# Performance work log

Hardware: AMD Instinct MI355X
Metric: run time of the kernel (lower is better)

The kernel has to match this reference:

```python
import jax, jax.numpy as jnp
import numpy as np

B, S, D = 4, 2048, 2048
H, K = 16, 128          # num_heads, intermediate_dim
FINAL = H * K           # 2048
VDIM = 2048             # vector_dim
EPS_LN = 1e-6
EPS_NORM = 1e-30


def setup_inputs() -> dict:
    key = jax.random.key(0)
    ks = jax.random.split(key, 8)
    x = jax.random.normal(ks[0], (B, S, D), dtype=jnp.float32)
    vector = jax.random.normal(ks[1], (B, VDIM), dtype=jnp.float32)
    W_att = jax.random.normal(ks[2], (D, H), dtype=jnp.float32) / np.sqrt(D)
    temperature = jnp.ones((1, 1, H), dtype=jnp.float32)
    W_values = jax.random.normal(ks[3], (D, H, K), dtype=jnp.float32) / np.sqrt(D)
    W_op = jax.random.normal(ks[4], (FINAL, VDIM), dtype=jnp.float32) / np.sqrt(FINAL)
    ff1 = jax.random.normal(ks[5], (VDIM + D, D), dtype=jnp.float32) / np.sqrt(VDIM + D)
    ff1_b = jnp.zeros((1, 1, D), dtype=jnp.float32)
    ff2 = jax.random.normal(ks[6], (D, D), dtype=jnp.float32) / np.sqrt(D)
    ff2_b = jnp.zeros((1, 1, D), dtype=jnp.float32)
    gamma = jnp.ones((D,), dtype=jnp.float32)
    beta = jnp.zeros((D,), dtype=jnp.float32)
    return {"x": x, "vector": vector, "W_att": W_att, "temperature": temperature,
            "W_values": W_values, "W_op": W_op, "ff1": ff1, "ff1_b": ff1_b,
            "ff2": ff2, "ff2_b": ff2_b, "gamma": gamma, "beta": beta}


def reference(x, vector, W_att, temperature, W_values, W_op, ff1, ff1_b, ff2, ff2_b, gamma, beta):
    b, s, d = x.shape
    # attention gate per (query) position -- [B,S,H]
    logits = jnp.matmul(x, W_att)
    logits = logits - jnp.max(logits, axis=-2, keepdims=True)
    w = jnp.exp(logits * temperature)
    # exact collapse of repeat+tril+normalize: A[b,i,j,h] = w[b,i,h]*tril[i,j]
    # denom[b,i,h] = w[b,i,h]*(i+1) + 1e-30  ->  out = coef * causal cumsum of v
    counts = jnp.arange(1, s + 1, dtype=x.dtype)[None, :, None]  # [1,S,1]
    coef = w / (w * counts + EPS_NORM)                            # [B,S,H]
    v = jnp.einsum('bsi,ihk->bshk', x, W_values)                  # [B,S,H,K]
    cum_v = jnp.cumsum(v, axis=1)                                 # prefix-sum over keys
    pooled = (coef[..., None] * cum_v).reshape(b, s, -1)          # [B,S,H*K]
    op = jnp.matmul(pooled, W_op) + vector[:, None, :]            # [B,S,VDIM]
    concat = jnp.concatenate([x, op], axis=-1)                    # [B,S,VDIM+D]
    h = jax.nn.relu(jnp.matmul(concat, ff1) + ff1_b)
    h = jax.nn.relu(jnp.matmul(h, ff2) + ff2_b)
    res = h + x
    mean = jnp.mean(res, axis=-1, keepdims=True)
    cen = res - mean
    var = jnp.mean(cen * cen, axis=-1, keepdims=True)
    return cen / jnp.sqrt(var + EPS_LN) * gamma + beta
```

## Files before the change

kernel.cpp:

```cpp
#include <hip/hip_runtime.h>
#include <stdint.h>

#define B_DIM 4
#define S_DIM 2048
#define D_DIM 2048
#define H_DIM 16
#define M_ROWS (B_DIM * S_DIM)
#define CONCAT_LD 4096
#define NCHUNK 32
#define CHLEN (S_DIM / NCHUNK)

#define BM 128
#define BN 128
#define BK 64

typedef __attribute__((ext_vector_type(8))) __bf16 bf16x8;
typedef __attribute__((ext_vector_type(4))) float f32x4;

__device__ inline unsigned short f2bf(float f) {
  union { float f; unsigned u; } x; x.f = f;
  unsigned r = x.u + 0x7fffu + ((x.u >> 16) & 1u);
  return (unsigned short)(r >> 16);
}
__device__ inline float bf2f(unsigned short s) {
  union { unsigned u; float f; } x; x.u = ((unsigned)s) << 16;
  return x.f;
}

__global__ __launch_bounds__(256) void xconv_logits_kernel(
    const float* __restrict__ x, const float* __restrict__ Watt,
    unsigned short* __restrict__ concat, float* __restrict__ logits) {
  int row = blockIdx.x, t = threadIdx.x;
  const float* xr = x + (size_t)row * D_DIM;
  unsigned short* cr = concat + (size_t)row * CONCAT_LD;
  float p[H_DIM];
#pragma unroll
  for (int h = 0; h < H_DIM; ++h) p[h] = 0.f;
#pragma unroll
  for (int i = 0; i < 8; ++i) {
    int k = t + i * 256;
    float xv = xr[k];
    cr[k] = f2bf(xv);
    const float* wr = Watt + (size_t)k * H_DIM;
#pragma unroll
    for (int h = 0; h < H_DIM; ++h) p[h] += xv * wr[h];
  }
  __shared__ float red[4][H_DIM];
  int l = t & 63, w = t >> 6;
#pragma unroll
  for (int h = 0; h < H_DIM; ++h) {
    float v = p[h];
    for (int off = 32; off; off >>= 1) v += __shfl_down(v, off);
    if (l == 0) red[w][h] = v;
  }
  __syncthreads();
  if (t < H_DIM)
    logits[(size_t)row * H_DIM + t] = red[0][t] + red[1][t] + red[2][t] + red[3][t];
}

__global__ __launch_bounds__(256) void transpose_conv_kernel(
    const float* __restrict__ src, unsigned short* __restrict__ dst, int R, int C) {
  __shared__ float tile[32][33];
  int c0 = blockIdx.x * 32, r0 = blockIdx.y * 32;
  int tx = threadIdx.x & 31, ty = threadIdx.x >> 5;
#pragma unroll
  for (int i = 0; i < 32; i += 8)
    tile[ty + i][tx] = src[(size_t)(r0 + ty + i) * C + c0 + tx];
  __syncthreads();
#pragma unroll
  for (int i = 0; i < 32; i += 8)
    dst[(size_t)(c0 + ty + i) * R + r0 + tx] = f2bf(tile[tx][ty + i]);
}

__global__ __launch_bounds__(256) void coef_kernel(
    const float* __restrict__ logits, const float* __restrict__ temp, float* __restrict__ coef) {
  int b = blockIdx.x >> 4, h = blockIdx.x & 15;
  int t = threadIdx.x;
  const float* lg = logits + (size_t)b * S_DIM * H_DIM + h;
  float mx = -1e30f;
  for (int s = t; s < S_DIM; s += 256) mx = fmaxf(mx, lg[(size_t)s * H_DIM]);
  for (int off = 32; off; off >>= 1) mx = fmaxf(mx, __shfl_down(mx, off));
  __shared__ float red[4];
  if ((t & 63) == 0) red[t >> 6] = mx;
  __syncthreads();
  mx = fmaxf(fmaxf(red[0], red[1]), fmaxf(red[2], red[3]));
  float T = temp[h];
  float* cf = coef + (size_t)b * S_DIM * H_DIM + h;
  for (int s = t; s < S_DIM; s += 256) {
    float w = expf((lg[(size_t)s * H_DIM] - mx) * T);
    cf[(size_t)s * H_DIM] = w / (w * (float)(s + 1) + 1e-30f);
  }
}

template <int MODE>
__global__ __launch_bounds__(256) void gemm_bt_kernel(
    const unsigned short* __restrict__ A, int lda,
    const unsigned short* __restrict__ Bt, int ldb, int K,
    void* __restrict__ outp, int ldo,
    const float* __restrict__ bias, const float* __restrict__ resid) {
  __shared__ unsigned short As[BM * BK];
  __shared__ unsigned short Bs[BN * BK];
  const int t = threadIdx.x;
  const int w = t >> 6, l = t & 63;
  const int wm = w & 1, wn = w >> 1;
  const int q = l >> 4, ln = l & 15;

  const int L = blockIdx.y * 16 + blockIdx.x;
  const int xcd = L & 7;
  const int W = L >> 3;
  const int bx = W & 15;
  const int by = (W >> 4) * 8 + xcd;
  const int m0 = by * BM, n0 = bx * BN;

  f32x4 acc[4][4];
#pragma unroll
  for (int i = 0; i < 4; ++i)
#pragma unroll
    for (int j = 0; j < 4; ++j) acc[i][j] = {0.f, 0.f, 0.f, 0.f};

  for (int k0 = 0; k0 < K; k0 += BK) {
    __syncthreads();
#pragma unroll
    for (int r = 0; r < 4; ++r) {
      int s = r * 256 + t;
      int row = s >> 3;
      int ch = (s & 7) ^ (row & 7);
      const unsigned short* ga = A + (size_t)(m0 + row) * lda + k0 + ch * 8;
      __builtin_amdgcn_global_load_lds(
          (const __attribute__((address_space(1))) void*)ga,
          (__attribute__((address_space(3))) void*)(As + (r * 256 + w * 64) * 8), 16, 0, 0);
      const unsigned short* gb = Bt + (size_t)(n0 + row) * ldb + k0 + ch * 8;
      __builtin_amdgcn_global_load_lds(
          (const __attribute__((address_space(1))) void*)gb,
          (__attribute__((address_space(3))) void*)(Bs + (r * 256 + w * 64) * 8), 16, 0, 0);
    }
    __syncthreads();
#pragma unroll
    for (int h = 0; h < 2; ++h) {
      bf16x8 af[4], bfr[4];
#pragma unroll
      for (int mt = 0; mt < 4; ++mt) {
        int ar = wm * 64 + mt * 16 + ln;
        af[mt] = *(const bf16x8*)&As[ar * BK + (((h * 4 + q) ^ (ar & 7)) * 8)];
      }
#pragma unroll
      for (int nt = 0; nt < 4; ++nt) {
        int br = wn * 64 + nt * 16 + ln;
        bfr[nt] = *(const bf16x8*)&Bs[br * BK + (((h * 4 + q) ^ (br & 7)) * 8)];
      }
#pragma unroll
      for (int mt = 0; mt < 4; ++mt)
#pragma unroll
        for (int nt = 0; nt < 4; ++nt)
          acc[mt][nt] = __builtin_amdgcn_mfma_f32_16x16x32_bf16(af[mt], bfr[nt], acc[mt][nt], 0, 0, 0);
    }
  }

#pragma unroll
  for (int mt = 0; mt < 4; ++mt) {
#pragma unroll
    for (int i = 0; i < 4; ++i) {
      int row = m0 + wm * 64 + mt * 16 + q * 4 + i;
#pragma unroll
      for (int nt = 0; nt < 4; ++nt) {
        int col = n0 + wn * 64 + nt * 16 + ln;
        float vv = acc[mt][nt][i];
        if (MODE == 2) vv += bias[(size_t)(row >> 11) * 2048 + col];
        if (MODE == 3) { vv += bias[col]; vv = fmaxf(vv, 0.f); }
        if (MODE == 4) {
          vv += bias[col]; vv = fmaxf(vv, 0.f);
          vv += resid[(size_t)row * 2048 + col];
          ((float*)outp)[(size_t)row * ldo + col] = vv;
        } else {
          ((unsigned short*)outp)[(size_t)row * ldo + col] = f2bf(vv);
        }
      }
    }
  }
}

__global__ __launch_bounds__(256) void scan_partial_kernel(
    const unsigned short* __restrict__ v, float* __restrict__ csum) {
  int c = blockIdx.x * 256 + threadIdx.x;
  int chunk = blockIdx.y, b = blockIdx.z;
  const unsigned short* p = v + ((size_t)(b * S_DIM + chunk * CHLEN)) * D_DIM + c;
  float s = 0.f;
#pragma unroll 4
  for (int i = 0; i < CHLEN; ++i) s += bf2f(p[(size_t)i * D_DIM]);
  csum[((size_t)b * NCHUNK + chunk) * D_DIM + c] = s;
}

__global__ __launch_bounds__(256) void scan_offsets_kernel(float* __restrict__ csum) {
  int c = blockIdx.x * 256 + threadIdx.x;
  int b = blockIdx.y;
  float run = 0.f;
  float* p = csum + (size_t)b * NCHUNK * D_DIM + c;
  for (int ch = 0; ch < NCHUNK; ++ch) {
    float tv = p[(size_t)ch * D_DIM];
    p[(size_t)ch * D_DIM] = run;
    run += tv;
  }
}

__global__ __launch_bounds__(256) void scan_apply_kernel(
    const unsigned short* __restrict__ v, const float* __restrict__ csum,
    const float* __restrict__ coef, unsigned short* __restrict__ pooled) {
  int c = blockIdx.x * 256 + threadIdx.x;
  int chunk = blockIdx.y, b = blockIdx.z;
  int h = c >> 7;
  float run = csum[((size_t)b * NCHUNK + chunk) * D_DIM + c];
  size_t base = ((size_t)(b * S_DIM + chunk * CHLEN)) * D_DIM + c;
  const float* cf = coef + ((size_t)b * S_DIM + chunk * CHLEN) * H_DIM + h;
#pragma unroll 4
  for (int i = 0; i < CHLEN; ++i) {
    run += bf2f(v[base + (size_t)i * D_DIM]);
    pooled[base + (size_t)i * D_DIM] = f2bf(cf[(size_t)i * H_DIM] * run);
  }
}

__global__ __launch_bounds__(256) void ln_kernel(
    float* __restrict__ out, const float* __restrict__ gamma, const float* __restrict__ beta) {
  int row = blockIdx.x, t = threadIdx.x;
  float* pr = out + (size_t)row * D_DIM;
  float vals[8];
  float s = 0.f;
#pragma unroll
  for (int i = 0; i < 8; ++i) { vals[i] = pr[t + i * 256]; s += vals[i]; }
  __shared__ float red[4];
  for (int off = 32; off; off >>= 1) s += __shfl_down(s, off);
  if ((t & 63) == 0) red[t >> 6] = s;
  __syncthreads();
  float mean = (red[0] + red[1] + red[2] + red[3]) * (1.f / D_DIM);
  __syncthreads();
  float c2 = 0.f;
#pragma unroll
  for (int i = 0; i < 8; ++i) { float c = vals[i] - mean; c2 += c * c; }
  for (int off = 32; off; off >>= 1) c2 += __shfl_down(c2, off);
  if ((t & 63) == 0) red[t >> 6] = c2;
  __syncthreads();
  float var = (red[0] + red[1] + red[2] + red[3]) * (1.f / D_DIM);
  float rstd = rsqrtf(var + 1e-6f);
#pragma unroll
  for (int i = 0; i < 8; ++i) {
    int col = t + i * 256;
    pr[col] = (vals[i] - mean) * rstd * gamma[col] + beta[col];
  }
}

extern "C" void kernel_launch(void* const* d_in, const int* in_sizes, int n_in,
                              void* d_out, int out_size, void* d_ws, size_t ws_size,
                              hipStream_t stream) {
  const float* x      = (const float*)d_in[0];
  const float* vector = (const float*)d_in[1];
  const float* W_att  = (const float*)d_in[2];
  const float* temp   = (const float*)d_in[3];
  const float* W_val  = (const float*)d_in[4];
  const float* W_op   = (const float*)d_in[5];
  const float* ff1    = (const float*)d_in[6];
  const float* ff1_b  = (const float*)d_in[7];
  const float* ff2    = (const float*)d_in[8];
  const float* ff2_b  = (const float*)d_in[9];
  const float* gamma  = (const float*)d_in[10];
  const float* beta   = (const float*)d_in[11];
  float* out = (float*)d_out;

  char* ws = (char*)d_ws;
  auto alloc = [&](size_t bytes) {
    char* p = ws; ws += (bytes + 255) & ~(size_t)255; return p;
  };
  unsigned short* concat = (unsigned short*)alloc((size_t)M_ROWS * CONCAT_LD * 2);
  unsigned short* wv_t   = (unsigned short*)alloc((size_t)2048 * 2048 * 2);
  unsigned short* wop_t  = (unsigned short*)alloc((size_t)2048 * 2048 * 2);
  unsigned short* ff1_t  = (unsigned short*)alloc((size_t)2048 * 4096 * 2);
  unsigned short* ff2_t  = (unsigned short*)alloc((size_t)2048 * 2048 * 2);
  unsigned short* vbuf   = (unsigned short*)alloc((size_t)M_ROWS * 2048 * 2);
  unsigned short* pooled = (unsigned short*)alloc((size_t)M_ROWS * 2048 * 2);
  unsigned short* h1     = (unsigned short*)alloc((size_t)M_ROWS * 2048 * 2);
  float* logits = (float*)alloc((size_t)M_ROWS * H_DIM * 4);
  float* coef   = (float*)alloc((size_t)M_ROWS * H_DIM * 4);
  float* csum   = (float*)alloc((size_t)B_DIM * NCHUNK * D_DIM * 4);

  xconv_logits_kernel<<<M_ROWS, 256, 0, stream>>>(x, W_att, concat, logits);
  transpose_conv_kernel<<<dim3(64, 64), 256, 0, stream>>>(W_val, wv_t, 2048, 2048);
  transpose_conv_kernel<<<dim3(64, 64), 256, 0, stream>>>(W_op, wop_t, 2048, 2048);
  transpose_conv_kernel<<<dim3(64, 128), 256, 0, stream>>>(ff1, ff1_t, 4096, 2048);
  transpose_conv_kernel<<<dim3(64, 64), 256, 0, stream>>>(ff2, ff2_t, 2048, 2048);
  coef_kernel<<<B_DIM * H_DIM, 256, 0, stream>>>(logits, temp, coef);
  gemm_bt_kernel<1><<<dim3(2048 / BN, M_ROWS / BM), 256, 0, stream>>>(
      concat, CONCAT_LD, wv_t, 2048, 2048, vbuf, 2048, nullptr, nullptr);
  scan_partial_kernel<<<dim3(8, NCHUNK, B_DIM), 256, 0, stream>>>(vbuf, csum);
  scan_offsets_kernel<<<dim3(8, B_DIM), 256, 0, stream>>>(csum);
  scan_apply_kernel<<<dim3(8, NCHUNK, B_DIM), 256, 0, stream>>>(vbuf, csum, coef, pooled);
  gemm_bt_kernel<2><<<dim3(2048 / BN, M_ROWS / BM), 256, 0, stream>>>(
      pooled, 2048, wop_t, 2048, 2048, concat + 2048, CONCAT_LD, vector, nullptr);
  gemm_bt_kernel<3><<<dim3(2048 / BN, M_ROWS / BM), 256, 0, stream>>>(
      concat, CONCAT_LD, ff1_t, 4096, 4096, h1, 2048, ff1_b, nullptr);
  gemm_bt_kernel<4><<<dim3(2048 / BN, M_ROWS / BM), 256, 0, stream>>>(
      h1, 2048, ff2_t, 2048, 2048, out, 2048, ff2_b, x);
  ln_kernel<<<M_ROWS, 256, 0, stream>>>(out, gamma, beta);
}
```

Before: 774.4 us.

## Fold W_op into ff1 and precompute the vector term as a per-batch bias

The op projection is folded into ff1 algebraically. A 2048x2048 weight-only GEMM computes W_op·ff1_bottom, and vector·ff1_bottom plus ff1_b becomes a per-batch bias. The pooled activations are written straight into the concat buffer, so the full-size op GEMM over 8192 rows goes away and one fewer large activation pass is needed. In exchange it adds a small weight-product GEMM each call and bf16 rounding of the fused weight, which may change numerics slightly.

```diff
diff --git a/kernel.cpp b/kernel.cpp
--- a/kernel.cpp
+++ b/kernel.cpp
@@ -59,7 +59,8 @@
 }
 
 __global__ __launch_bounds__(256) void transpose_conv_kernel(
-    const float* __restrict__ src, unsigned short* __restrict__ dst, int R, int C) {
+    const float* __restrict__ src, unsigned short* __restrict__ dst,
+    int R, int C, int ldd) {
   __shared__ float tile[32][33];
   int c0 = blockIdx.x * 32, r0 = blockIdx.y * 32;
   int tx = threadIdx.x & 31, ty = threadIdx.x >> 5;
@@ -69,7 +70,16 @@
   __syncthreads();
 #pragma unroll
   for (int i = 0; i < 32; i += 8)
-    dst[(size_t)(c0 + ty + i) * R + r0 + tx] = f2bf(tile[tx][ty + i]);
+    dst[(size_t)(c0 + ty + i) * ldd + r0 + tx] = f2bf(tile[tx][ty + i]);
+}
+
+__global__ __launch_bounds__(256) void convert_kernel(
+    const float* __restrict__ src, unsigned short* __restrict__ dst) {
+  int idx = (blockIdx.x * 256 + threadIdx.x) * 4;
+  const float4 v = *(const float4*)(src + idx);
+  ushort4 o;
+  o.x = f2bf(v.x); o.y = f2bf(v.y); o.z = f2bf(v.z); o.w = f2bf(v.w);
+  *(ushort4*)(dst + idx) = o;
 }
 
 __global__ __launch_bounds__(256) void coef_kernel(
@@ -90,6 +100,30 @@
     float w = expf((lg[(size_t)s * H_DIM] - mx) * T);
     cf[(size_t)s * H_DIM] = w / (w * (float)(s + 1) + 1e-30f);
   }
+}
+
+__global__ __launch_bounds__(256) void bias2_partial_kernel(
+    const float* __restrict__ vector, const float* __restrict__ ff1,
+    float* __restrict__ part) {
+  int n = blockIdx.x * 256 + threadIdx.x;
+  int seg = blockIdx.y, b = blockIdx.z;
+  const float* vr = vector + (size_t)b * 2048 + seg * 128;
+  const float* fr = ff1 + (size_t)(2048 + seg * 128) * 2048 + n;
+  float acc = 0.f;
+#pragma unroll 8
+  for (int j = 0; j < 128; ++j) acc += vr[j] * fr[(size_t)j * 2048];
+  part[((size_t)seg * 4 + b) * 2048 + n] = acc;
+}
+
+__global__ __launch_bounds__(256) void bias2_reduce_kernel(
+    const float* __restrict__ part, const float* __restrict__ ff1_b,
+    float* __restrict__ bias2) {
+  int n = blockIdx.x * 256 + threadIdx.x;
+  int b = blockIdx.y;
+  float acc = ff1_b[n];
+#pragma unroll
+  for (int s = 0; s < 16; ++s) acc += part[((size_t)s * 4 + b) * 2048 + n];
+  bias2[(size_t)b * 2048 + n] = acc;
 }
 
 template <int MODE>
@@ -165,8 +199,7 @@
       for (int nt = 0; nt < 4; ++nt) {
         int col = n0 + wn * 64 + nt * 16 + ln;
         float vv = acc[mt][nt][i];
-        if (MODE == 2) vv += bias[(size_t)(row >> 11) * 2048 + col];
-        if (MODE == 3) { vv += bias[col]; vv = fmaxf(vv, 0.f); }
+        if (MODE == 2) { vv += bias[(size_t)(row >> 11) * 2048 + col]; vv = fmaxf(vv, 0.f); }
         if (MODE == 4) {
           vv += bias[col]; vv = fmaxf(vv, 0.f);
           vv += resid[(size_t)row * 2048 + col];
@@ -204,17 +237,19 @@
 
 __global__ __launch_bounds__(256) void scan_apply_kernel(
     const unsigned short* __restrict__ v, const float* __restrict__ csum,
-    const float* __restrict__ coef, unsigned short* __restrict__ pooled) {
+    const float* __restrict__ coef, unsigned short* __restrict__ pooled_out) {
   int c = blockIdx.x * 256 + threadIdx.x;
   int chunk = blockIdx.y, b = blockIdx.z;
   int h = c >> 7;
+  int row0 = b * S_DIM + chunk * CHLEN;
   float run = csum[((size_t)b * NCHUNK + chunk) * D_DIM + c];
-  size_t base = ((size_t)(b * S_DIM + chunk * CHLEN)) * D_DIM + c;
-  const float* cf = coef + ((size_t)b * S_DIM + chunk * CHLEN) * H_DIM + h;
+  const unsigned short* vp = v + (size_t)row0 * D_DIM + c;
+  unsigned short* po = pooled_out + (size_t)row0 * CONCAT_LD + c;
+  const float* cf = coef + (size_t)row0 * H_DIM + h;
 #pragma unroll 4
   for (int i = 0; i < CHLEN; ++i) {
-    run += bf2f(v[base + (size_t)i * D_DIM]);
-    pooled[base + (size_t)i * D_DIM] = f2bf(cf[(size_t)i * H_DIM] * run);
+    run += bf2f(vp[(size_t)i * D_DIM]);
+    po[(size_t)i * CONCAT_LD] = f2bf(cf[(size_t)i * H_DIM] * run);
   }
 }
 
@@ -270,32 +305,37 @@
   };
   unsigned short* concat = (unsigned short*)alloc((size_t)M_ROWS * CONCAT_LD * 2);
   unsigned short* wv_t   = (unsigned short*)alloc((size_t)2048 * 2048 * 2);
-  unsigned short* wop_t  = (unsigned short*)alloc((size_t)2048 * 2048 * 2);
-  unsigned short* ff1_t  = (unsigned short*)alloc((size_t)2048 * 4096 * 2);
+  unsigned short* btff1  = (unsigned short*)alloc((size_t)2048 * 4096 * 2);
+  unsigned short* f1bT   = (unsigned short*)alloc((size_t)2048 * 2048 * 2);
+  unsigned short* wop_bf = (unsigned short*)alloc((size_t)2048 * 2048 * 2);
   unsigned short* ff2_t  = (unsigned short*)alloc((size_t)2048 * 2048 * 2);
   unsigned short* vbuf   = (unsigned short*)alloc((size_t)M_ROWS * 2048 * 2);
-  unsigned short* pooled = (unsigned short*)alloc((size_t)M_ROWS * 2048 * 2);
   unsigned short* h1     = (unsigned short*)alloc((size_t)M_ROWS * 2048 * 2);
   float* logits = (float*)alloc((size_t)M_ROWS * H_DIM * 4);
   float* coef   = (float*)alloc((size_t)M_ROWS * H_DIM * 4);
   float* csum   = (float*)alloc((size_t)B_DIM * NCHUNK * D_DIM * 4);
+  float* part   = (float*)alloc((size_t)16 * 4 * 2048 * 4);
+  float* bias2  = (float*)alloc((size_t)4 * 2048 * 4);
 
   xconv_logits_kernel<<<M_ROWS, 256, 0, stream>>>(x, W_att, concat, logits);
-  transpose_conv_kernel<<<dim3(64, 64), 256, 0, stream>>>(W_val, wv_t, 2048, 2048);
-  transpose_conv_kernel<<<dim3(64, 64), 256, 0, stream>>>(W_op, wop_t, 2048, 2048);
-  transpose_conv_kernel<<<dim3(64, 128), 256, 0, stream>>>(ff1, ff1_t, 4096, 2048);
-  transpose_conv_kernel<<<dim3(64, 64), 256, 0, stream>>>(ff2, ff2_t, 2048, 2048);
+  transpose_conv_kernel<<<dim3(64, 64), 256, 0, stream>>>(W_val, wv_t, 2048, 2048, 2048);
+  transpose_conv_kernel<<<dim3(64, 64), 256, 0, stream>>>(ff1, btff1, 2048, 2048, 4096);
+  transpose_conv_kernel<<<dim3(64, 64), 256, 0, stream>>>(ff1 + (size_t)2048 * 2048, f1bT, 2048, 2048, 2048);
+  convert_kernel<<<2048 * 2048 / 1024, 256, 0, stream>>>(W_op, wop_bf);
+  transpose_conv_kernel<<<dim3(64, 64), 256, 0, stream>>>(ff2, ff2_t, 2048, 2048, 2048);
   coef_kernel<<<B_DIM * H_DIM, 256, 0, stream>>>(logits, temp, coef);
-  gemm_bt_kernel<1><<<dim3(2048 / BN, M_ROWS / BM), 256, 0, stream>>>(
+  gemm_bt_kernel<1><<<dim3(16, 16), 256, 0, stream>>>(
+      f1bT, 2048, wop_bf, 2048, 2048, btff1 + 2048, 4096, nullptr, nullptr);
+  bias2_partial_kernel<<<dim3(8, 16, 4), 256, 0, stream>>>(vector, ff1, part);
+  bias2_reduce_kernel<<<dim3(8, 4), 256, 0, stream>>>(part, ff1_b, bias2);
+  gemm_bt_kernel<1><<<dim3(16, 64), 256, 0, stream>>>(
       concat, CONCAT_LD, wv_t, 2048, 2048, vbuf, 2048, nullptr, nullptr);
   scan_partial_kernel<<<dim3(8, NCHUNK, B_DIM), 256, 0, stream>>>(vbuf, csum);
   scan_offsets_kernel<<<dim3(8, B_DIM), 256, 0, stream>>>(csum);
-  scan_apply_kernel<<<dim3(8, NCHUNK, B_DIM), 256, 0, stream>>>(vbuf, csum, coef, pooled);
-  gemm_bt_kernel<2><<<dim3(2048 / BN, M_ROWS / BM), 256, 0, stream>>>(
-      pooled, 2048, wop_t, 2048, 2048, concat + 2048, CONCAT_LD, vector, nullptr);
-  gemm_bt_kernel<3><<<dim3(2048 / BN, M_ROWS / BM), 256, 0, stream>>>(
-      concat, CONCAT_LD, ff1_t, 4096, 4096, h1, 2048, ff1_b, nullptr);
-  gemm_bt_kernel<4><<<dim3(2048 / BN, M_ROWS / BM), 256, 0, stream>>>(
+  scan_apply_kernel<<<dim3(8, NCHUNK, B_DIM), 256, 0, stream>>>(vbuf, csum, coef, concat + 2048);
+  gemm_bt_kernel<2><<<dim3(16, 64), 256, 0, stream>>>(
+      concat, CONCAT_LD, btff1, 4096, 4096, h1, 2048, bias2, nullptr);
+  gemm_bt_kernel<4><<<dim3(16, 64), 256, 0, stream>>>(
       h1, 2048, ff2_t, 2048, 2048, out, 2048, ff2_b, x);
   ln_kernel<<<M_ROWS, 256, 0, stream>>>(out, gamma, beta);
 }
```

Result: faster. 737.9 us (-4.7%).
